# Kernel optimization log

Hardware: AMD Instinct MI355X
Metric: run time of the kernel (lower is better)

The kernel has to match this reference:

```python
import jax, jax.numpy as jnp
import numpy as np

OUT = 7          # out_size
SCALE = 0.125    # spatial_scale (1/8, FPN P3)
SAMPLES = 2      # sample_num


def setup_inputs() -> dict:
    key = jax.random.key(0)
    k1, k2, k3, k4, k5, k6, k7, k8, k9 = jax.random.split(key, 9)
    B, C, H, W = 2, 256, 256, 256
    n = 1024
    features = jax.random.normal(k1, (B, C, H, W), jnp.float32)
    # rois: (batch_idx, cx, cy, w, h, theta) in IMAGE coordinates
    bidx = jax.random.randint(k2, (n,), 0, B).astype(jnp.float32)
    cx = jax.random.uniform(k3, (n,), jnp.float32, 0.0, W / SCALE)
    cy = jax.random.uniform(k4, (n,), jnp.float32, 0.0, H / SCALE)
    rw = jax.random.uniform(k5, (n,), jnp.float32, 16.0, 512.0)
    rh = jax.random.uniform(k6, (n,), jnp.float32, 16.0, 512.0)
    ang = jax.random.uniform(k7, (n,), jnp.float32, -np.pi, np.pi)
    rois = jnp.stack([bidx, cx, cy, rw, rh, ang], axis=1)
    ic = OUT * OUT * C  # 12544
    fc = 1024
    w1 = jax.random.normal(k8, (ic, fc), jnp.float32) * 0.01
    b1 = jnp.zeros((fc,), jnp.float32)
    w2 = jax.random.normal(k9, (fc, OUT * OUT), jnp.float32) * 0.01
    b2 = jnp.zeros((OUT * OUT,), jnp.float32)
    return {"features": features, "rois": rois, "w1": w1, "b1": b1, "w2": w2, "b2": b2}


def _roi_align_rotated(features, rois):
    B, C, H, W = features.shape
    n = rois.shape[0]
    bidx = rois[:, 0].astype(jnp.int32)
    cx = rois[:, 1] * SCALE
    cy = rois[:, 2] * SCALE
    rw = jnp.maximum(rois[:, 3] * SCALE, 1.0)
    rh = jnp.maximum(rois[:, 4] * SCALE, 1.0)
    theta = rois[:, 5]
    bin_w = rw / OUT
    bin_h = rh / OUT
    g = jnp.arange(OUT, dtype=features.dtype)
    s = (jnp.arange(SAMPLES, dtype=features.dtype) + 0.5) / SAMPLES
    # roi-local sample coordinates: [n, OUT, SAMPLES]
    yy = -rh[:, None, None] / 2 + (g[None, :, None] + s[None, None, :]) * bin_h[:, None, None]
    xx = -rw[:, None, None] / 2 + (g[None, :, None] + s[None, None, :]) * bin_w[:, None, None]
    # broadcast to [n, oh, ow, sy, sx]
    yy = yy[:, :, None, :, None]
    xx = xx[:, None, :, None, :]
    ct = jnp.cos(theta)[:, None, None, None, None]
    st = jnp.sin(theta)[:, None, None, None, None]
    xs = xx * ct - yy * st + cx[:, None, None, None, None]
    ys = xx * st + yy * ct + cy[:, None, None, None, None]
    shp = (n, OUT, OUT, SAMPLES, SAMPLES)
    xs = jnp.broadcast_to(xs, shp).reshape(n, -1)  # [n, P], P = OUT*OUT*S*S
    ys = jnp.broadcast_to(ys, shp).reshape(n, -1)
    valid = (ys > -1.0) & (ys < H) & (xs > -1.0) & (xs < W)
    ysc = jnp.clip(ys, 0.0, H - 1)
    xsc = jnp.clip(xs, 0.0, W - 1)
    yl = jnp.floor(ysc).astype(jnp.int32)
    xl = jnp.floor(xsc).astype(jnp.int32)
    yh = jnp.minimum(yl + 1, H - 1)
    xh = jnp.minimum(xl + 1, W - 1)
    ly = ysc - yl
    lx = xsc - xl
    hy = 1.0 - ly
    hx = 1.0 - lx
    be = jnp.broadcast_to(bidx[:, None], yl.shape)
    # bilinear gathers: each [n, P, C]
    v11 = features[be, :, yl, xl]
    v12 = features[be, :, yl, xh]
    v21 = features[be, :, yh, xl]
    v22 = features[be, :, yh, xh]
    val = ((hy * hx)[..., None] * v11 + (hy * lx)[..., None] * v12
           + (ly * hx)[..., None] * v21 + (ly * lx)[..., None] * v22)
    val = val * valid[..., None].astype(val.dtype)
    # average the SAMPLES*SAMPLES points per bin -> [n, OUT, OUT, C]
    val = val.reshape(n, OUT, OUT, SAMPLES * SAMPLES, C).mean(axis=3)
    return jnp.transpose(val, (0, 3, 1, 2))  # [n, C, OUT, OUT]


def reference(features, rois, w1, b1, w2, b2):
    n = rois.shape[0]
    x = _roi_align_rotated(features, rois)          # [n, C, OUT, OUT]
    flat = x.reshape(n, -1)                          # [n, C*OUT*OUT]
    hid = jax.nn.relu(flat @ w1 + b1)
    mask = jax.nn.sigmoid(hid @ w2 + b2).reshape(n, 1, OUT, OUT)
    return x * mask
```

## Files before the change

kernel.cpp:

```cpp
#include <hip/hip_runtime.h>
#include <hip/hip_bf16.h>

typedef unsigned short u16;
typedef short short8 __attribute__((ext_vector_type(8)));
typedef float f32x4 __attribute__((ext_vector_type(4)));

#define OUTD 7
#define NROI 1024
#define CH 256
#define KDIM 12544
#define NHID 1024
#define KSPLIT 8

__device__ __forceinline__ float bf2f(u16 u) {
    union { unsigned int i; float f; } v; v.i = ((unsigned int)u) << 16; return v.f;
}
__device__ __forceinline__ u16 f2b(float f) {
    return (u16)(__bfloat16_as_ushort(__float2bfloat16(f)));
}

__global__ __launch_bounds__(256) void transpose_feat(const float* __restrict__ f,
                                                      u16* __restrict__ ft) {
    __shared__ float tile[32][129];
    int pb = blockIdx.x;
    int cb = blockIdx.y;
    int b  = blockIdx.z;
    int tid = threadIdx.x;
    const float* src = f + ((size_t)(b * CH + cb * 32)) * 65536 + (size_t)pb * 128;
#pragma unroll
    for (int i = 0; i < 4; ++i) {
        int id = tid + 256 * i;
        int c = id >> 5, f4 = id & 31;
        float4 v = *(const float4*)(src + (size_t)c * 65536 + f4 * 4);
        tile[c][f4 * 4 + 0] = v.x;
        tile[c][f4 * 4 + 1] = v.y;
        tile[c][f4 * 4 + 2] = v.z;
        tile[c][f4 * 4 + 3] = v.w;
    }
    __syncthreads();
    u16* dst = ft + ((size_t)(b * 65536 + pb * 128)) * CH + cb * 32;
#pragma unroll
    for (int i = 0; i < 4; ++i) {
        int id = tid + 256 * i;
        int px = id >> 3, cg = id & 7;
        uint2 o;
        o.x = (unsigned)f2b(tile[cg * 4 + 0][px]) | ((unsigned)f2b(tile[cg * 4 + 1][px]) << 16);
        o.y = (unsigned)f2b(tile[cg * 4 + 2][px]) | ((unsigned)f2b(tile[cg * 4 + 3][px]) << 16);
        *(uint2*)(dst + (size_t)px * CH + cg * 4) = o;
    }
}

__global__ __launch_bounds__(256) void transpose_w1(const float* __restrict__ w1,
                                                    u16* __restrict__ w1t) {
    __shared__ float tile[32][129];
    int kb = blockIdx.x;
    int nb = blockIdx.y;
    int tid = threadIdx.x;
#pragma unroll
    for (int i = 0; i < 4; ++i) {
        int id = tid + 256 * i;
        int r = id >> 3, f4 = id & 7;
        float4 v = *(const float4*)(w1 + (size_t)(kb * 128 + r) * NHID + nb * 32 + f4 * 4);
        tile[f4 * 4 + 0][r] = v.x;
        tile[f4 * 4 + 1][r] = v.y;
        tile[f4 * 4 + 2][r] = v.z;
        tile[f4 * 4 + 3][r] = v.w;
    }
    __syncthreads();
#pragma unroll
    for (int i = 0; i < 4; ++i) {
        int id = tid + 256 * i;
        int nn = id >> 5, kg = id & 31;
        uint2 o;
        o.x = (unsigned)f2b(tile[nn][kg * 4 + 0]) | ((unsigned)f2b(tile[nn][kg * 4 + 1]) << 16);
        o.y = (unsigned)f2b(tile[nn][kg * 4 + 2]) | ((unsigned)f2b(tile[nn][kg * 4 + 3]) << 16);
        *(uint2*)(w1t + (size_t)(nb * 32 + nn) * KDIM + kb * 128 + kg * 4) = o;
    }
}

__global__ __launch_bounds__(256) void roi_align(const u16* __restrict__ ft,
                                                 const float* __restrict__ rois,
                                                 float* __restrict__ x,
                                                 u16* __restrict__ flat) {
    __shared__ float sbuf[49 * 257];
    int i = blockIdx.x;
    int tid = threadIdx.x;
    int lane = tid & 63, w = tid >> 6;
    float r0 = rois[i * 6 + 0], r1 = rois[i * 6 + 1], r2 = rois[i * 6 + 2];
    float r3 = rois[i * 6 + 3], r4 = rois[i * 6 + 4], th = rois[i * 6 + 5];
    int b = (int)r0;
    float cx = r1 * 0.125f, cy = r2 * 0.125f;
    float rw = fmaxf(r3 * 0.125f, 1.0f), rh = fmaxf(r4 * 0.125f, 1.0f);
    float bw = rw * (1.0f / 7.0f), bh = rh * (1.0f / 7.0f);
    float ct = cosf(th), st = sinf(th);
    const u16* fb = ft + (size_t)b * 65536 * CH;
    int coff = lane * 4;

    int start = w * 12 + (w > 0 ? 1 : 0);
    int cnt = (w == 0) ? 13 : 12;
    for (int bi = 0; bi < cnt; ++bi) {
        int bin = start + bi;
        int ph = bin / 7, pw = bin - ph * 7;
        float a0 = 0.f, a1 = 0.f, a2 = 0.f, a3 = 0.f;
#pragma unroll
        for (int s = 0; s < 4; ++s) {
            int sy = s >> 1, sx2 = s & 1;
            float yy = -rh * 0.5f + ((float)ph + ((float)sy + 0.5f) * 0.5f) * bh;
            float xx = -rw * 0.5f + ((float)pw + ((float)sx2 + 0.5f) * 0.5f) * bw;
            float xs = xx * ct - yy * st + cx;
            float ys = xx * st + yy * ct + cy;
            bool valid = (ys > -1.0f) && (ys < 256.0f) && (xs > -1.0f) && (xs < 256.0f);
            float ysc = fminf(fmaxf(ys, 0.f), 255.f);
            float xsc = fminf(fmaxf(xs, 0.f), 255.f);
            int yl = (int)floorf(ysc), xl = (int)floorf(xsc);
            int yh = min(yl + 1, 255), xh = min(xl + 1, 255);
            float ly = ysc - (float)yl, lx = xsc - (float)xl;
            float hy = 1.f - ly, hx = 1.f - lx;
            float w11 = hy * hx, w12 = hy * lx, w21 = ly * hx, w22 = ly * lx;
            if (!valid) { w11 = w12 = w21 = w22 = 0.f; }
            uint2 v11 = *(const uint2*)(fb + (((size_t)yl * 256 + xl) << 8) + coff);
            uint2 v12 = *(const uint2*)(fb + (((size_t)yl * 256 + xh) << 8) + coff);
            uint2 v21 = *(const uint2*)(fb + (((size_t)yh * 256 + xl) << 8) + coff);
            uint2 v22 = *(const uint2*)(fb + (((size_t)yh * 256 + xh) << 8) + coff);
            a0 += w11 * bf2f(v11.x & 0xffff) + w12 * bf2f(v12.x & 0xffff)
                + w21 * bf2f(v21.x & 0xffff) + w22 * bf2f(v22.x & 0xffff);
            a1 += w11 * bf2f(v11.x >> 16)    + w12 * bf2f(v12.x >> 16)
                + w21 * bf2f(v21.x >> 16)    + w22 * bf2f(v22.x >> 16);
            a2 += w11 * bf2f(v11.y & 0xffff) + w12 * bf2f(v12.y & 0xffff)
                + w21 * bf2f(v21.y & 0xffff) + w22 * bf2f(v22.y & 0xffff);
            a3 += w11 * bf2f(v11.y >> 16)    + w12 * bf2f(v12.y >> 16)
                + w21 * bf2f(v21.y >> 16)    + w22 * bf2f(v22.y >> 16);
        }
        float* sb = sbuf + bin * 257 + coff;
        sb[0] = a0 * 0.25f; sb[1] = a1 * 0.25f; sb[2] = a2 * 0.25f; sb[3] = a3 * 0.25f;
    }
    __syncthreads();
    size_t base = (size_t)i * KDIM;
#pragma unroll 1
    for (int k = 0; k < 49; ++k) {
        int o = tid + k * 256;
        int c = o / 49, bin = o - c * 49;
        float v = sbuf[bin * 257 + c];
        x[base + o] = v;
        flat[base + o] = f2b(v);
    }
}

__global__ __launch_bounds__(256) void gemm1(const u16* __restrict__ A,
                                             const u16* __restrict__ Bt,
                                             float* __restrict__ part) {
    const int K = KDIM;
    int nb = blockIdx.x, mb = blockIdx.y, ks = blockIdx.z;
    int steps = 24 + (ks < 4 ? 1 : 0);
    int kbase = (ks * 24 + (ks < 4 ? ks : 4)) * 64;
    __shared__ u16 As[128 * 64];
    __shared__ u16 Bs[128 * 64];
    int tid = threadIdx.x;
    int lane = tid & 63, w = tid >> 6;
    int wm = w >> 1, wn = w & 1;
    f32x4 acc[4][4] = {};
    const u16* Ab = A + (size_t)(mb * 128) * K;
    const u16* Bb = Bt + (size_t)(nb * 128) * K;

    for (int s = 0; s < steps; ++s) {
        int kk = kbase + s * 64;
        __syncthreads();
#pragma unroll
        for (int j = 0; j < 4; ++j) {
            int cid = tid + 256 * j;
            int row = cid >> 3, pq = cid & 7;
            int q = pq ^ (row & 7);
            uint4 va = *(const uint4*)(Ab + (size_t)row * K + kk + q * 8);
            *(uint4*)(As + row * 64 + pq * 8) = va;
            uint4 vb = *(const uint4*)(Bb + (size_t)row * K + kk + q * 8);
            *(uint4*)(Bs + row * 64 + pq * 8) = vb;
        }
        __syncthreads();
#pragma unroll
        for (int kh = 0; kh < 2; ++kh) {
            short8 af[4], bf[4];
#pragma unroll
            for (int t = 0; t < 4; ++t) {
                int q = kh * 4 + (lane >> 4);
                int r = wm * 64 + t * 16 + (lane & 15);
                int pq = q ^ (r & 7);
                af[t] = *(const short8*)(As + r * 64 + pq * 8);
                int rb = wn * 64 + t * 16 + (lane & 15);
                int pqb = q ^ (rb & 7);
                bf[t] = *(const short8*)(Bs + rb * 64 + pqb * 8);
            }
#pragma unroll
            for (int mt = 0; mt < 4; ++mt)
#pragma unroll
                for (int nt = 0; nt < 4; ++nt)
                    acc[mt][nt] = __builtin_amdgcn_mfma_f32_16x16x32_bf16(af[mt], bf[nt], acc[mt][nt], 0, 0, 0);
        }
    }
    float* P = part + (size_t)ks * NROI * NHID;
    int m_base = mb * 128 + wm * 64, n_base = nb * 128 + wn * 64;
#pragma unroll
    for (int mt = 0; mt < 4; ++mt)
#pragma unroll
        for (int nt = 0; nt < 4; ++nt)
#pragma unroll
            for (int i = 0; i < 4; ++i) {
                int m = m_base + mt * 16 + (lane >> 4) * 4 + i;
                int n = n_base + nt * 16 + (lane & 15);
                P[(size_t)m * NHID + n] = acc[mt][nt][i];
            }
}

__global__ __launch_bounds__(256) void reduce_relu(const float* __restrict__ part,
                                                   const float* __restrict__ b1,
                                                   float* __restrict__ hid) {
    int idx4 = blockIdx.x * 256 + threadIdx.x;
    const float4* pv = (const float4*)part;
    const float4* bv = (const float4*)b1;
    float4 s = bv[idx4 & 255];
#pragma unroll
    for (int j = 0; j < KSPLIT; ++j) {
        float4 p = pv[(size_t)j * 262144 + idx4];
        s.x += p.x; s.y += p.y; s.z += p.z; s.w += p.w;
    }
    float4 r;
    r.x = fmaxf(s.x, 0.f); r.y = fmaxf(s.y, 0.f);
    r.z = fmaxf(s.z, 0.f); r.w = fmaxf(s.w, 0.f);
    ((float4*)hid)[idx4] = r;
}

__global__ __launch_bounds__(64) void gemm2_mask(const float* __restrict__ hid,
                                                 const float* __restrict__ w2,
                                                 const float* __restrict__ b2,
                                                 float* __restrict__ mask) {
    __shared__ float hrow[NHID];
    int i = blockIdx.x;
    for (int k = threadIdx.x; k < NHID; k += 64) hrow[k] = hid[(size_t)i * NHID + k];
    __syncthreads();
    int j = threadIdx.x;
    if (j < 49) {
        float acc = b2[j];
        for (int k = 0; k < NHID; ++k) acc += hrow[k] * w2[(size_t)k * 49 + j];
        mask[i * 49 + j] = 1.f / (1.f + expf(-acc));
    }
}

__global__ __launch_bounds__(256) void apply_mask(float* __restrict__ out,
                                                  const float* __restrict__ mask) {
    __shared__ float mrow[49];
    int i = blockIdx.x;
    int tid = threadIdx.x;
    if (tid < 49) mrow[tid] = mask[i * 49 + tid];
    __syncthreads();
    float4* o = (float4*)(out + (size_t)i * KDIM);
#pragma unroll 1
    for (int idx = tid; idx < 3136; idx += 256) {
        float4 v = o[idx];
        int e = idx * 4;
        int p = e % 49;
        v.x *= mrow[p]; if (++p == 49) p = 0;
        v.y *= mrow[p]; if (++p == 49) p = 0;
        v.z *= mrow[p]; if (++p == 49) p = 0;
        v.w *= mrow[p];
        o[idx] = v;
    }
}

extern "C" void kernel_launch(void* const* d_in, const int* in_sizes, int n_in,
                              void* d_out, int out_size, void* d_ws, size_t ws_size,
                              hipStream_t stream) {
    const float* features = (const float*)d_in[0];
    const float* rois     = (const float*)d_in[1];
    const float* w1       = (const float*)d_in[2];
    const float* b1       = (const float*)d_in[3];
    const float* w2       = (const float*)d_in[4];
    const float* b2       = (const float*)d_in[5];
    float* out = (float*)d_out;
    char* ws = (char*)d_ws;

    u16* featT  = (u16*)(ws);
    u16* flat   = (u16*)(ws + 67108864);
    u16* w1t    = (u16*)(ws + 92798976);
    float* part = (float*)(ws + 118489088);
    float* hid  = (float*)(ws + 152043520);
    float* mask = (float*)(ws + 156237824);

    transpose_feat<<<dim3(512, 8, 2), 256, 0, stream>>>(features, featT);
    transpose_w1<<<dim3(98, 32), 256, 0, stream>>>(w1, w1t);
    roi_align<<<NROI, 256, 0, stream>>>(featT, rois, out, flat);
    gemm1<<<dim3(8, 8, KSPLIT), 256, 0, stream>>>(flat, w1t, part);
    reduce_relu<<<1024, 256, 0, stream>>>(part, b1, hid);
    gemm2_mask<<<NROI, 64, 0, stream>>>(hid, w2, b2, mask);
    apply_mask<<<NROI, 256, 0, stream>>>(out, mask);
}
```

Baseline: 417.8 us.

## Fuse mask GEMM with apply, async LDS loads in gemm1, bf16 roi output

roi_align now writes only the bf16 flat buffer, no longer the fp32 x output. The final output is rebuilt from bf16 values times the mask in a fused gemm2+apply kernel, which also uses a transposed w2 and spreads the dot products over 245 threads. gemm1 switches its tile loads to global_load_lds direct-to-LDS copies. These cut global memory traffic and a launch, but the output now carries bf16 rounding instead of fp32 precision.

```diff
diff --git a/kernel.cpp b/kernel.cpp
--- a/kernel.cpp
+++ b/kernel.cpp
@@ -2,6 +2,7 @@
 #include <hip/hip_bf16.h>
 
 typedef unsigned short u16;
+typedef unsigned int u32;
 typedef short short8 __attribute__((ext_vector_type(8)));
 typedef float f32x4 __attribute__((ext_vector_type(4)));
 
@@ -12,11 +13,18 @@
 #define NHID 1024
 #define KSPLIT 8
 
-__device__ __forceinline__ float bf2f(u16 u) {
-    union { unsigned int i; float f; } v; v.i = ((unsigned int)u) << 16; return v.f;
+__device__ __forceinline__ float bf_lo(u32 u) {
+    union { u32 i; float f; } v; v.i = u << 16; return v.f;
+}
+__device__ __forceinline__ float bf_hi(u32 u) {
+    union { u32 i; float f; } v; v.i = u & 0xffff0000u; return v.f;
 }
 __device__ __forceinline__ u16 f2b(float f) {
     return (u16)(__bfloat16_as_ushort(__float2bfloat16(f)));
+}
+__device__ __forceinline__ void async16(const void* g, void* l) {
+    __builtin_amdgcn_global_load_lds((const __attribute__((address_space(1))) u32*)g,
+                                     (__attribute__((address_space(3))) u32*)l, 16, 0, 0);
 }
 
 __global__ __launch_bounds__(256) void transpose_feat(const float* __restrict__ f,
@@ -44,8 +52,8 @@
         int id = tid + 256 * i;
         int px = id >> 3, cg = id & 7;
         uint2 o;
-        o.x = (unsigned)f2b(tile[cg * 4 + 0][px]) | ((unsigned)f2b(tile[cg * 4 + 1][px]) << 16);
-        o.y = (unsigned)f2b(tile[cg * 4 + 2][px]) | ((unsigned)f2b(tile[cg * 4 + 3][px]) << 16);
+        o.x = (u32)f2b(tile[cg * 4 + 0][px]) | ((u32)f2b(tile[cg * 4 + 1][px]) << 16);
+        o.y = (u32)f2b(tile[cg * 4 + 2][px]) | ((u32)f2b(tile[cg * 4 + 3][px]) << 16);
         *(uint2*)(dst + (size_t)px * CH + cg * 4) = o;
     }
 }
@@ -72,17 +80,23 @@
         int id = tid + 256 * i;
         int nn = id >> 5, kg = id & 31;
         uint2 o;
-        o.x = (unsigned)f2b(tile[nn][kg * 4 + 0]) | ((unsigned)f2b(tile[nn][kg * 4 + 1]) << 16);
-        o.y = (unsigned)f2b(tile[nn][kg * 4 + 2]) | ((unsigned)f2b(tile[nn][kg * 4 + 3]) << 16);
+        o.x = (u32)f2b(tile[nn][kg * 4 + 0]) | ((u32)f2b(tile[nn][kg * 4 + 1]) << 16);
+        o.y = (u32)f2b(tile[nn][kg * 4 + 2]) | ((u32)f2b(tile[nn][kg * 4 + 3]) << 16);
         *(uint2*)(w1t + (size_t)(nb * 32 + nn) * KDIM + kb * 128 + kg * 4) = o;
     }
+}
+
+__global__ __launch_bounds__(256) void transpose_w2(const float* __restrict__ w2,
+                                                    float* __restrict__ w2t) {
+    int j = blockIdx.x;
+    for (int k = threadIdx.x; k < NHID; k += 256)
+        w2t[(size_t)j * NHID + k] = w2[(size_t)k * 49 + j];
 }
 
 __global__ __launch_bounds__(256) void roi_align(const u16* __restrict__ ft,
                                                  const float* __restrict__ rois,
-                                                 float* __restrict__ x,
                                                  u16* __restrict__ flat) {
-    __shared__ float sbuf[49 * 257];
+    __shared__ u16 sbuf[49 * 260];
     int i = blockIdx.x;
     int tid = threadIdx.x;
     int lane = tid & 63, w = tid >> 6;
@@ -122,27 +136,30 @@
             uint2 v12 = *(const uint2*)(fb + (((size_t)yl * 256 + xh) << 8) + coff);
             uint2 v21 = *(const uint2*)(fb + (((size_t)yh * 256 + xl) << 8) + coff);
             uint2 v22 = *(const uint2*)(fb + (((size_t)yh * 256 + xh) << 8) + coff);
-            a0 += w11 * bf2f(v11.x & 0xffff) + w12 * bf2f(v12.x & 0xffff)
-                + w21 * bf2f(v21.x & 0xffff) + w22 * bf2f(v22.x & 0xffff);
-            a1 += w11 * bf2f(v11.x >> 16)    + w12 * bf2f(v12.x >> 16)
-                + w21 * bf2f(v21.x >> 16)    + w22 * bf2f(v22.x >> 16);
-            a2 += w11 * bf2f(v11.y & 0xffff) + w12 * bf2f(v12.y & 0xffff)
-                + w21 * bf2f(v21.y & 0xffff) + w22 * bf2f(v22.y & 0xffff);
-            a3 += w11 * bf2f(v11.y >> 16)    + w12 * bf2f(v12.y >> 16)
-                + w21 * bf2f(v21.y >> 16)    + w22 * bf2f(v22.y >> 16);
+            a0 += w11 * bf_lo(v11.x) + w12 * bf_lo(v12.x) + w21 * bf_lo(v21.x) + w22 * bf_lo(v22.x);
+            a1 += w11 * bf_hi(v11.x) + w12 * bf_hi(v12.x) + w21 * bf_hi(v21.x) + w22 * bf_hi(v22.x);
+            a2 += w11 * bf_lo(v11.y) + w12 * bf_lo(v12.y) + w21 * bf_lo(v21.y) + w22 * bf_lo(v22.y);
+            a3 += w11 * bf_hi(v11.y) + w12 * bf_hi(v12.y) + w21 * bf_hi(v21.y) + w22 * bf_hi(v22.y);
         }
-        float* sb = sbuf + bin * 257 + coff;
-        sb[0] = a0 * 0.25f; sb[1] = a1 * 0.25f; sb[2] = a2 * 0.25f; sb[3] = a3 * 0.25f;
-    }
-    __syncthreads();
-    size_t base = (size_t)i * KDIM;
+        uint2 o;
+        o.x = (u32)f2b(a0 * 0.25f) | ((u32)f2b(a1 * 0.25f) << 16);
+        o.y = (u32)f2b(a2 * 0.25f) | ((u32)f2b(a3 * 0.25f) << 16);
+        *(uint2*)(sbuf + bin * 260 + coff) = o;
+    }
+    __syncthreads();
+    uint2* fl = (uint2*)(flat + (size_t)i * KDIM);
 #pragma unroll 1
-    for (int k = 0; k < 49; ++k) {
-        int o = tid + k * 256;
-        int c = o / 49, bin = o - c * 49;
-        float v = sbuf[bin * 257 + c];
-        x[base + o] = v;
-        flat[base + o] = f2b(v);
+    for (int k = tid; k < 3136; k += 256) {
+        int e = k * 4;
+        int c = e / 49, bn = e - c * 49;
+        u16 r0_ = sbuf[bn * 260 + c]; if (++bn == 49) { bn = 0; ++c; }
+        u16 r1_ = sbuf[bn * 260 + c]; if (++bn == 49) { bn = 0; ++c; }
+        u16 r2_ = sbuf[bn * 260 + c]; if (++bn == 49) { bn = 0; ++c; }
+        u16 r3_ = sbuf[bn * 260 + c];
+        uint2 o;
+        o.x = (u32)r0_ | ((u32)r1_ << 16);
+        o.y = (u32)r2_ | ((u32)r3_ << 16);
+        fl[k] = o;
     }
 }
 
@@ -167,13 +184,12 @@
         __syncthreads();
 #pragma unroll
         for (int j = 0; j < 4; ++j) {
-            int cid = tid + 256 * j;
+            int c = w * 4 + j;
+            int cid = c * 64 + lane;
             int row = cid >> 3, pq = cid & 7;
             int q = pq ^ (row & 7);
-            uint4 va = *(const uint4*)(Ab + (size_t)row * K + kk + q * 8);
-            *(uint4*)(As + row * 64 + pq * 8) = va;
-            uint4 vb = *(const uint4*)(Bb + (size_t)row * K + kk + q * 8);
-            *(uint4*)(Bs + row * 64 + pq * 8) = vb;
+            async16(Ab + (size_t)row * K + kk + q * 8, As + c * 512 + lane * 8);
+            async16(Bb + (size_t)row * K + kk + q * 8, Bs + c * 512 + lane * 8);
         }
         __syncthreads();
 #pragma unroll
@@ -228,40 +244,51 @@
     ((float4*)hid)[idx4] = r;
 }
 
-__global__ __launch_bounds__(64) void gemm2_mask(const float* __restrict__ hid,
-                                                 const float* __restrict__ w2,
-                                                 const float* __restrict__ b2,
-                                                 float* __restrict__ mask) {
-    __shared__ float hrow[NHID];
-    int i = blockIdx.x;
-    for (int k = threadIdx.x; k < NHID; k += 64) hrow[k] = hid[(size_t)i * NHID + k];
-    __syncthreads();
-    int j = threadIdx.x;
-    if (j < 49) {
-        float acc = b2[j];
-        for (int k = 0; k < NHID; ++k) acc += hrow[k] * w2[(size_t)k * 49 + j];
-        mask[i * 49 + j] = 1.f / (1.f + expf(-acc));
-    }
-}
-
-__global__ __launch_bounds__(256) void apply_mask(float* __restrict__ out,
-                                                  const float* __restrict__ mask) {
+__global__ __launch_bounds__(256) void gemm2_apply(const float* __restrict__ hid,
+                                                   const float* __restrict__ w2t,
+                                                   const float* __restrict__ b2,
+                                                   const u16* __restrict__ flat,
+                                                   float* __restrict__ out) {
+    __shared__ __align__(16) float hrow[NHID];
+    __shared__ float partial[256];
     __shared__ float mrow[49];
     int i = blockIdx.x;
     int tid = threadIdx.x;
-    if (tid < 49) mrow[tid] = mask[i * 49 + tid];
-    __syncthreads();
-    float4* o = (float4*)(out + (size_t)i * KDIM);
+    for (int k = tid; k < NHID; k += 256) hrow[k] = hid[(size_t)i * NHID + k];
+    __syncthreads();
+    float p = 0.f;
+    if (tid < 245) {
+        int j = tid / 5, kc = tid - (tid / 5) * 5;
+        int k0 = (256 * kc) / 5, k1 = (256 * (kc + 1)) / 5;
+        const float4* wv = (const float4*)(w2t + (size_t)j * NHID);
+        const float4* hv = (const float4*)hrow;
+        for (int k = k0; k < k1; ++k) {
+            float4 a = hv[k], b = wv[k];
+            p += a.x * b.x + a.y * b.y + a.z * b.z + a.w * b.w;
+        }
+    }
+    partial[tid] = p;
+    __syncthreads();
+    if (tid < 49) {
+        float s = b2[tid];
+#pragma unroll
+        for (int q = 0; q < 5; ++q) s += partial[tid * 5 + q];
+        mrow[tid] = 1.f / (1.f + expf(-s));
+    }
+    __syncthreads();
+    const uint2* fl = (const uint2*)(flat + (size_t)i * KDIM);
+    float4* op = (float4*)(out + (size_t)i * KDIM);
 #pragma unroll 1
     for (int idx = tid; idx < 3136; idx += 256) {
-        float4 v = o[idx];
+        uint2 v = fl[idx];
         int e = idx * 4;
-        int p = e % 49;
-        v.x *= mrow[p]; if (++p == 49) p = 0;
-        v.y *= mrow[p]; if (++p == 49) p = 0;
-        v.z *= mrow[p]; if (++p == 49) p = 0;
-        v.w *= mrow[p];
-        o[idx] = v;
+        int pp = e - (e / 49) * 49;
+        float4 r;
+        r.x = bf_lo(v.x) * mrow[pp]; if (++pp == 49) pp = 0;
+        r.y = bf_hi(v.x) * mrow[pp]; if (++pp == 49) pp = 0;
+        r.z = bf_lo(v.y) * mrow[pp]; if (++pp == 49) pp = 0;
+        r.w = bf_hi(v.y) * mrow[pp];
+        op[idx] = r;
     }
 }
 
@@ -282,13 +309,13 @@
     u16* w1t    = (u16*)(ws + 92798976);
     float* part = (float*)(ws + 118489088);
     float* hid  = (float*)(ws + 152043520);
-    float* mask = (float*)(ws + 156237824);
+    float* w2t  = (float*)(ws + 156237824);
 
     transpose_feat<<<dim3(512, 8, 2), 256, 0, stream>>>(features, featT);
     transpose_w1<<<dim3(98, 32), 256, 0, stream>>>(w1, w1t);
-    roi_align<<<NROI, 256, 0, stream>>>(featT, rois, out, flat);
+    transpose_w2<<<49, 256, 0, stream>>>(w2, w2t);
+    roi_align<<<NROI, 256, 0, stream>>>(featT, rois, flat);
     gemm1<<<dim3(8, 8, KSPLIT), 256, 0, stream>>>(flat, w1t, part);
     reduce_relu<<<1024, 256, 0, stream>>>(part, b1, hid);
-    gemm2_mask<<<NROI, 64, 0, stream>>>(hid, w2, b2, mask);
-    apply_mask<<<NROI, 256, 0, stream>>>(out, mask);
-}
+    gemm2_apply<<<NROI, 256, 0, stream>>>(hid, w2t, b2, flat, out);
+}
```

Result: faster. 386.7 us (-7.4%).
